# Performance work log

Measured on AMD Instinct MI355X. Metric: run time of the kernel, lower is better.

Reference implementation:

```python
import jax, jax.numpy as jnp
import numpy as np

SIZE_IN = 4096
SIZE_OUT = 8192
EPS = 1e-8  # torch.cosine_similarity default eps


def setup_inputs() -> dict:
    key = jax.random.key(0)
    kx, kw = jax.random.split(key)
    x = jax.random.normal(kx, (4096, SIZE_IN), dtype=jnp.float32)
    # kaiming_uniform_(a=sqrt(5)) -> uniform(-bound, bound), bound = sqrt(6/((1+a^2)*fan_in)) = 1/sqrt(fan_in)
    bound = 1.0 / np.sqrt(SIZE_IN)
    weights = jax.random.uniform(kw, (SIZE_OUT, SIZE_IN), dtype=jnp.float32,
                                 minval=-bound, maxval=bound)
    return {"x": x, "weights": weights}


def reference(x, weights):
    # cosine similarity of each row of x with each weight row, done as one GEMM
    # out[b, o] = <x[b], w[o]> / (max(||x[b]||, eps) * max(||w[o]||, eps))
    x_norm = jnp.maximum(jnp.linalg.norm(x, axis=-1, keepdims=True), EPS)     # [B,1]
    w_norm = jnp.maximum(jnp.linalg.norm(weights, axis=-1), EPS)              # [O]
    dots = jnp.einsum('bi,oi->bo', x, weights)                                # [B,O]
    return dots / (x_norm * w_norm[None, :])
```

## Files before the change

### kernel.cpp

```cpp
#include <hip/hip_runtime.h>
#include <hip/hip_bf16.h>
#include <stdint.h>

#define M_DIM 4096
#define N_DIM 8192
#define K_DIM 4096
#define EPS_F 1e-8f

typedef __attribute__((ext_vector_type(8))) _Float16 f16x8;
typedef __attribute__((ext_vector_type(4))) _Float16 f16x4;
typedef __attribute__((ext_vector_type(4))) float f32x4;

#define GLD16(g, l) __builtin_amdgcn_global_load_lds( \
    (const __attribute__((address_space(1))) void*)(g), \
    (__attribute__((address_space(3))) void*)(l), 16, 0, 0)

#define BARRIER() do { asm volatile("" ::: "memory"); \
  __builtin_amdgcn_s_barrier(); asm volatile("" ::: "memory"); } while (0)

__global__ __launch_bounds__(256) void prep_kernel(
    const float* __restrict__ x, const float* __restrict__ w,
    _Float16* __restrict__ xh, _Float16* __restrict__ wh,
    float* __restrict__ partials) {
  int r = blockIdx.x;
  const float* src;
  _Float16* dst;
  if (r < M_DIM) {
    src = x + (size_t)r * K_DIM;
    dst = xh + (size_t)r * K_DIM;
  } else {
    int rr = r - M_DIM;
    src = w + (size_t)rr * K_DIM;
    dst = wh + (size_t)rr * K_DIM;
  }
  const int lane = threadIdx.x & 63;
  const int wv = threadIdx.x >> 6;
  const int base = wv * 1024;
  float s = 0.f;
#pragma unroll
  for (int i = 0; i < 4; ++i) {
    int c = base + i * 256 + lane * 4;
    float4 v = *(const float4*)(src + c);
    s += v.x * v.x + v.y * v.y + v.z * v.z + v.w * v.w;
    f16x4 h;
    h[0] = (_Float16)v.x; h[1] = (_Float16)v.y;
    h[2] = (_Float16)v.z; h[3] = (_Float16)v.w;
    *(f16x4*)(dst + c) = h;
  }
#pragma unroll
  for (int off = 32; off > 0; off >>= 1) s += __shfl_down(s, off);
  if (lane == 0) partials[r * 4 + wv] = s;
}

__global__ __launch_bounds__(256) void finalize_kernel(
    const float* __restrict__ partials,
    float* __restrict__ rxn, float* __restrict__ rwn) {
  int r = blockIdx.x * 256 + threadIdx.x;
  f32x4 p = *(const f32x4*)(partials + (size_t)r * 4);
  float t = p[0] + p[1] + p[2] + p[3];
  float v = 1.0f / fmaxf(sqrtf(t), EPS_F);
  if (r < M_DIM) rxn[r] = v;
  else rwn[r - M_DIM] = v;
}

__global__ __launch_bounds__(512, 2) void gemm_cos_kernel(
    const _Float16* __restrict__ xh, const _Float16* __restrict__ wh,
    const float* __restrict__ rxn, const float* __restrict__ rwn,
    float* __restrict__ out) {
  __shared__ __align__(16) char lds[131072];

  const int tid = threadIdx.x;
  const int lane = tid & 63;
  const int wid = tid >> 6;
  const int wm = wid >> 2;
  const int wn = wid & 3;

  int bid = blockIdx.x;
  int swz = (bid & 7) * 64 + (bid >> 3);
  const int bm = (swz >> 5) << 8;
  const int bn = (swz & 31) << 8;

  const int srow = tid >> 2;
  const int scsrc = (tid & 3) ^ ((srow >> 1) & 3);
  const size_t a0_off = (size_t)(bm + srow) * K_DIM + scsrc * 8;
  const size_t a1_off = (size_t)(bm + 128 + srow) * K_DIM + scsrc * 8;
  const size_t b0_off = (size_t)(bn + srow) * K_DIM + scsrc * 8;
  const size_t b1_off = (size_t)(bn + 128 + srow) * K_DIM + scsrc * 8;

  char* const lds_my = lds + tid * 16;

  const int j16 = lane >> 4;
  const int arow_base = wm * 128 + (lane & 15);
  const int brow_base = wn * 64 + (lane & 15);

  f32x4 acc[8][4] = {};

  const int NT = K_DIM / 32;

#define STAGE_A(s) do { int s_ = (s); \
    size_t kt_ = (size_t)s_ * 32; \
    char* d_ = lds_my + (size_t)(s_ & 3) * 32768; \
    GLD16(xh + a0_off + kt_, d_); \
    GLD16(xh + a1_off + kt_, d_ + 8192); } while (0)

#define STAGE_B(s) do { int s_ = (s); \
    size_t kt_ = (size_t)s_ * 32; \
    char* d_ = lds_my + (size_t)(s_ & 3) * 32768; \
    GLD16(wh + b0_off + kt_, d_ + 16384); \
    GLD16(wh + b1_off + kt_, d_ + 24576); } while (0)

  STAGE_A(0); STAGE_B(0);
  STAGE_A(1); STAGE_B(1);
  STAGE_A(2); STAGE_B(2);
  asm volatile("s_waitcnt vmcnt(8)" ::: "memory");
  BARRIER();

  for (int T = 0; T < NT; ++T) {
    char* buf = lds + (size_t)(T & 3) * 32768;
    const bool stg = (T + 3 < NT);

    f16x8 af[4], bg[4];

#pragma unroll
    for (int mi = 0; mi < 4; ++mi) {
      int r = arow_base + mi * 16;
      af[mi] = *(const f16x8*)(buf + r * 64 + ((j16 ^ ((r >> 1) & 3)) << 4));
    }
#pragma unroll
    for (int ni = 0; ni < 4; ++ni) {
      int r = brow_base + ni * 16;
      bg[ni] = *(const f16x8*)(buf + 16384 + r * 64 +
                               ((j16 ^ ((r >> 1) & 3)) << 4));
    }
    if (stg) STAGE_A(T + 3);
    BARRIER();
    __builtin_amdgcn_s_setprio(1);
#pragma unroll
    for (int mi = 0; mi < 4; ++mi)
#pragma unroll
      for (int ni = 0; ni < 4; ++ni)
        acc[mi][ni] = __builtin_amdgcn_mfma_f32_16x16x32_f16(
            af[mi], bg[ni], acc[mi][ni], 0, 0, 0);
    __builtin_amdgcn_s_setprio(0);
    BARRIER();

#pragma unroll
    for (int mi = 0; mi < 4; ++mi) {
      int r = arow_base + 64 + mi * 16;
      af[mi] = *(const f16x8*)(buf + r * 64 + ((j16 ^ ((r >> 1) & 3)) << 4));
    }
    if (stg) STAGE_B(T + 3);
    BARRIER();
    __builtin_amdgcn_s_setprio(1);
#pragma unroll
    for (int mi = 0; mi < 4; ++mi)
#pragma unroll
      for (int ni = 0; ni < 4; ++ni)
        acc[4 + mi][ni] = __builtin_amdgcn_mfma_f32_16x16x32_f16(
            af[mi], bg[ni], acc[4 + mi][ni], 0, 0, 0);
    __builtin_amdgcn_s_setprio(0);

    if (T < NT - 3) {
      asm volatile("s_waitcnt vmcnt(8)" ::: "memory");
    } else if (T == NT - 3) {
      asm volatile("s_waitcnt vmcnt(4)" ::: "memory");
    } else if (T == NT - 2) {
      asm volatile("s_waitcnt vmcnt(0)" ::: "memory");
    }
    BARRIER();
  }

  const int ocol = bn + wn * 64 + (lane & 15);
  const int orow0 = bm + wm * 128 + ((lane >> 4) << 2);
  float rw[4];
#pragma unroll
  for (int ni = 0; ni < 4; ++ni) rw[ni] = rwn[ocol + ni * 16];
#pragma unroll
  for (int m = 0; m < 8; ++m) {
#pragma unroll
    for (int jj = 0; jj < 4; ++jj) {
      int r = orow0 + m * 16 + jj;
      float rx = rxn[r];
#pragma unroll
      for (int ni = 0; ni < 4; ++ni)
        out[(size_t)r * N_DIM + ocol + ni * 16] = acc[m][ni][jj] * rx * rw[ni];
    }
  }
#undef STAGE_A
#undef STAGE_B
}

__global__ __launch_bounds__(256) void fb_norms_kernel(
    const float* __restrict__ x, const float* __restrict__ w,
    float* __restrict__ rxn, float* __restrict__ rwn) {
  int r = blockIdx.x;
  const float* src = (r < M_DIM) ? x + (size_t)r * K_DIM
                                 : w + (size_t)(r - M_DIM) * K_DIM;
  float* rn = (r < M_DIM) ? rxn + r : rwn + (r - M_DIM);
  int tid = threadIdx.x;
  float s = 0.f;
#pragma unroll
  for (int i = 0; i < 4; ++i) {
    int c = (i * 256 + tid) * 4;
    float4 v = *(const float4*)(src + c);
    s += v.x * v.x + v.y * v.y + v.z * v.z + v.w * v.w;
  }
#pragma unroll
  for (int off = 32; off > 0; off >>= 1) s += __shfl_down(s, off);
  __shared__ float red[4];
  if ((tid & 63) == 0) red[tid >> 6] = s;
  __syncthreads();
  if (tid == 0) {
    float t = red[0] + red[1] + red[2] + red[3];
    *rn = 1.0f / fmaxf(sqrtf(t), EPS_F);
  }
}

__global__ __launch_bounds__(256) void fb_gemm_kernel(
    const float* __restrict__ x, const float* __restrict__ w,
    const float* __restrict__ rxn, const float* __restrict__ rwn,
    float* __restrict__ out) {
  __shared__ float As[64][17];
  __shared__ float Bs[64][17];
  int bm = blockIdx.y * 64, bn = blockIdx.x * 64;
  int tid = threadIdx.x;
  int tx = tid & 15, ty = tid >> 4;
  float acc[4][4] = {};
  for (int kt = 0; kt < K_DIM; kt += 16) {
#pragma unroll
    for (int i = 0; i < 4; ++i) {
      int e = i * 256 + tid;
      As[e >> 4][e & 15] = x[(size_t)(bm + (e >> 4)) * K_DIM + kt + (e & 15)];
      Bs[e >> 4][e & 15] = w[(size_t)(bn + (e >> 4)) * K_DIM + kt + (e & 15)];
    }
    __syncthreads();
#pragma unroll
    for (int k = 0; k < 16; ++k)
#pragma unroll
      for (int mi = 0; mi < 4; ++mi)
#pragma unroll
        for (int ni = 0; ni < 4; ++ni)
          acc[mi][ni] += As[ty * 4 + mi][k] * Bs[tx * 4 + ni][k];
    __syncthreads();
  }
#pragma unroll
  for (int mi = 0; mi < 4; ++mi) {
    int r = bm + ty * 4 + mi;
    float rx = rxn[r];
#pragma unroll
    for (int ni = 0; ni < 4; ++ni) {
      int c = bn + tx * 4 + ni;
      out[(size_t)r * N_DIM + c] = acc[mi][ni] * rx * rwn[c];
    }
  }
}

extern "C" void kernel_launch(void* const* d_in, const int* in_sizes, int n_in,
                              void* d_out, int out_size, void* d_ws, size_t ws_size,
                              hipStream_t stream) {
  const float* x = (const float*)d_in[0];
  const float* w = (const float*)d_in[1];
  float* out = (float*)d_out;
  char* ws = (char*)d_ws;

  float* rxn = (float*)ws;
  float* rwn = (float*)(ws + (16 << 10));
  float* partials = (float*)(ws + (64 << 10));
  const size_t base = 256 << 10;
  const size_t xelems = (size_t)M_DIM * K_DIM;
  const size_t welems = (size_t)N_DIM * K_DIM;
  const size_t need = base + (xelems + welems) * sizeof(_Float16);

  if (ws_size >= need) {
    _Float16* xh = (_Float16*)(ws + base);
    _Float16* wh = xh + xelems;
    prep_kernel<<<M_DIM + N_DIM, 256, 0, stream>>>(x, w, xh, wh, partials);
    finalize_kernel<<<(M_DIM + N_DIM) / 256, 256, 0, stream>>>(partials, rxn,
                                                               rwn);
    gemm_cos_kernel<<<512, 512, 0, stream>>>(xh, wh, rxn, rwn, out);
  } else {
    fb_norms_kernel<<<M_DIM + N_DIM, 256, 0, stream>>>(x, w, rxn, rwn);
    fb_gemm_kernel<<<dim3(N_DIM / 64, M_DIM / 64), 256, 0, stream>>>(
        x, w, rxn, rwn, out);
  }
}
```

Before: 528.5 us.

## Restructure GEMM main loop into double-buffered 64-wide K tiles with half-step staging

The K loop now processes 64-wide K tiles in two LDS buffers, each split into two 32-wide halves, instead of a 4-deep ring of 32-wide tiles. Global-to-LDS loads for the next tile are issued in quarter pieces across four compute phases, with explicit lgkmcnt waits and sched_barriers before each MFMA block. The aim is to halve loop overhead and vmcnt waits per K element and give the scheduler a fixed order of LDS reads versus MFMAs. The trade-off is a shallower prefetch distance and more barriers per iteration, which could expose memory latency.

Result: no change. 524.4 us (-0.8%).

```diff
diff --git a/kernel.cpp b/kernel.cpp
--- a/kernel.cpp
+++ b/kernel.cpp
@@ -81,93 +81,145 @@
   const int bn = (swz & 31) << 8;
 
   const int srow = tid >> 2;
-  const int scsrc = (tid & 3) ^ ((srow >> 1) & 3);
-  const size_t a0_off = (size_t)(bm + srow) * K_DIM + scsrc * 8;
-  const size_t a1_off = (size_t)(bm + 128 + srow) * K_DIM + scsrc * 8;
-  const size_t b0_off = (size_t)(bn + srow) * K_DIM + scsrc * 8;
-  const size_t b1_off = (size_t)(bn + 128 + srow) * K_DIM + scsrc * 8;
-
-  char* const lds_my = lds + tid * 16;
+  const int jg = (tid & 3) ^ ((tid >> 3) & 3);
+  const size_t aoff0 = (size_t)(bm + srow) * K_DIM + jg * 8;
+  const size_t aoff1 = (size_t)(bm + 128 + srow) * K_DIM + jg * 8;
+  const size_t boff0 = (size_t)(bn + srow) * K_DIM + jg * 8;
+  const size_t boff1 = (size_t)(bn + 128 + srow) * K_DIM + jg * 8;
 
   const int j16 = lane >> 4;
-  const int arow_base = wm * 128 + (lane & 15);
-  const int brow_base = wn * 64 + (lane & 15);
+  const int arb = wm * 128 + (lane & 15);
+  const int brb = wn * 64 + (lane & 15);
 
   f32x4 acc[8][4] = {};
-
-  const int NT = K_DIM / 32;
-
-#define STAGE_A(s) do { int s_ = (s); \
-    size_t kt_ = (size_t)s_ * 32; \
-    char* d_ = lds_my + (size_t)(s_ & 3) * 32768; \
-    GLD16(xh + a0_off + kt_, d_); \
-    GLD16(xh + a1_off + kt_, d_ + 8192); } while (0)
-
-#define STAGE_B(s) do { int s_ = (s); \
-    size_t kt_ = (size_t)s_ * 32; \
-    char* d_ = lds_my + (size_t)(s_ & 3) * 32768; \
-    GLD16(wh + b0_off + kt_, d_ + 16384); \
-    GLD16(wh + b1_off + kt_, d_ + 24576); } while (0)
-
-  STAGE_A(0); STAGE_B(0);
-  STAGE_A(1); STAGE_B(1);
-  STAGE_A(2); STAGE_B(2);
-  asm volatile("s_waitcnt vmcnt(8)" ::: "memory");
+  const int NT = K_DIM / 64;
+
+#define STAGE(ptr, off0, off1, s_, ks_, isB) do { \
+    char* d_ = lds + (size_t)((s_) & 1) * 65536 + (isB) * 32768 + \
+               (ks_) * 16384 + tid * 16; \
+    size_t g_ = (size_t)(s_) * 64 + (ks_) * 32; \
+    GLD16(ptr + off0 + g_, d_); \
+    GLD16(ptr + off1 + g_, d_ + 8192); } while (0)
+
+#define LDSWZ(base_, r_) ((base_) + (r_) * 64 + ((j16 ^ (((r_) >> 1) & 3)) << 4))
+
+  STAGE(xh, aoff0, aoff1, 0, 0, 0);
+  STAGE(wh, boff0, boff1, 0, 0, 1);
+  STAGE(xh, aoff0, aoff1, 0, 1, 0);
+  STAGE(wh, boff0, boff1, 0, 1, 1);
+  STAGE(xh, aoff0, aoff1, 1, 0, 0);
+  STAGE(wh, boff0, boff1, 1, 0, 1);
+  asm volatile("s_waitcnt vmcnt(4)" ::: "memory");
   BARRIER();
 
   for (int T = 0; T < NT; ++T) {
-    char* buf = lds + (size_t)(T & 3) * 32768;
-    const bool stg = (T + 3 < NT);
-
+    char* const bufb = lds + (size_t)(T & 1) * 65536;
     f16x8 af[4], bg[4];
 
-#pragma unroll
-    for (int mi = 0; mi < 4; ++mi) {
-      int r = arow_base + mi * 16;
-      af[mi] = *(const f16x8*)(buf + r * 64 + ((j16 ^ ((r >> 1) & 3)) << 4));
-    }
-#pragma unroll
-    for (int ni = 0; ni < 4; ++ni) {
-      int r = brow_base + ni * 16;
-      bg[ni] = *(const f16x8*)(buf + 16384 + r * 64 +
-                               ((j16 ^ ((r >> 1) & 3)) << 4));
-    }
-    if (stg) STAGE_A(T + 3);
-    BARRIER();
-    __builtin_amdgcn_s_setprio(1);
-#pragma unroll
-    for (int mi = 0; mi < 4; ++mi)
-#pragma unroll
-      for (int ni = 0; ni < 4; ++ni)
-        acc[mi][ni] = __builtin_amdgcn_mfma_f32_16x16x32_f16(
-            af[mi], bg[ni], acc[mi][ni], 0, 0, 0);
-    __builtin_amdgcn_s_setprio(0);
-    BARRIER();
-
-#pragma unroll
-    for (int mi = 0; mi < 4; ++mi) {
-      int r = arow_base + 64 + mi * 16;
-      af[mi] = *(const f16x8*)(buf + r * 64 + ((j16 ^ ((r >> 1) & 3)) << 4));
-    }
-    if (stg) STAGE_B(T + 3);
-    BARRIER();
-    __builtin_amdgcn_s_setprio(1);
-#pragma unroll
-    for (int mi = 0; mi < 4; ++mi)
-#pragma unroll
-      for (int ni = 0; ni < 4; ++ni)
-        acc[4 + mi][ni] = __builtin_amdgcn_mfma_f32_16x16x32_f16(
-            af[mi], bg[ni], acc[4 + mi][ni], 0, 0, 0);
-    __builtin_amdgcn_s_setprio(0);
-
-    if (T < NT - 3) {
-      asm volatile("s_waitcnt vmcnt(8)" ::: "memory");
-    } else if (T == NT - 3) {
-      asm volatile("s_waitcnt vmcnt(4)" ::: "memory");
-    } else if (T == NT - 2) {
-      asm volatile("s_waitcnt vmcnt(0)" ::: "memory");
-    }
-    BARRIER();
+    {
+      char* ab = bufb;
+      char* bb = bufb + 32768;
+#pragma unroll
+      for (int mi = 0; mi < 4; ++mi) {
+        int r = arb + mi * 16;
+        af[mi] = *(const f16x8*)LDSWZ(ab, r);
+      }
+#pragma unroll
+      for (int ni = 0; ni < 4; ++ni) {
+        int r = brb + ni * 16;
+        bg[ni] = *(const f16x8*)LDSWZ(bb, r);
+      }
+      if (T + 1 < NT) STAGE(xh, aoff0, aoff1, T + 1, 1, 0);
+      BARRIER();
+      asm volatile("s_waitcnt lgkmcnt(0)" ::: "memory");
+      __builtin_amdgcn_sched_barrier(0);
+      __builtin_amdgcn_s_setprio(1);
+#pragma unroll
+      for (int mi = 0; mi < 4; ++mi)
+#pragma unroll
+        for (int ni = 0; ni < 4; ++ni)
+          acc[mi][ni] = __builtin_amdgcn_mfma_f32_16x16x32_f16(
+              af[mi], bg[ni], acc[mi][ni], 0, 0, 0);
+      __builtin_amdgcn_s_setprio(0);
+      BARRIER();
+    }
+
+    {
+      char* ab = bufb;
+#pragma unroll
+      for (int mi = 0; mi < 4; ++mi) {
+        int r = arb + 64 + mi * 16;
+        af[mi] = *(const f16x8*)LDSWZ(ab, r);
+      }
+      if (T + 1 < NT) STAGE(wh, boff0, boff1, T + 1, 1, 1);
+      BARRIER();
+      asm volatile("s_waitcnt lgkmcnt(0)" ::: "memory");
+      __builtin_amdgcn_sched_barrier(0);
+      __builtin_amdgcn_s_setprio(1);
+#pragma unroll
+      for (int mi = 0; mi < 4; ++mi)
+#pragma unroll
+        for (int ni = 0; ni < 4; ++ni)
+          acc[4 + mi][ni] = __builtin_amdgcn_mfma_f32_16x16x32_f16(
+              af[mi], bg[ni], acc[4 + mi][ni], 0, 0, 0);
+      __builtin_amdgcn_s_setprio(0);
+      BARRIER();
+    }
+
+    {
+      char* ab = bufb + 16384;
+      char* bb = bufb + 49152;
+#pragma unroll
+      for (int mi = 0; mi < 4; ++mi) {
+        int r = arb + mi * 16;
+        af[mi] = *(const f16x8*)LDSWZ(ab, r);
+      }
+#pragma unroll
+      for (int ni = 0; ni < 4; ++ni) {
+        int r = brb + ni * 16;
+        bg[ni] = *(const f16x8*)LDSWZ(bb, r);
+      }
+      if (T + 2 < NT) STAGE(xh, aoff0, aoff1, T + 2, 0, 0);
+      BARRIER();
+      asm volatile("s_waitcnt lgkmcnt(0)" ::: "memory");
+      __builtin_amdgcn_sched_barrier(0);
+      __builtin_amdgcn_s_setprio(1);
+#pragma unroll
+      for (int mi = 0; mi < 4; ++mi)
+#pragma unroll
+        for (int ni = 0; ni < 4; ++ni)
+          acc[mi][ni] = __builtin_amdgcn_mfma_f32_16x16x32_f16(
+              af[mi], bg[ni], acc[mi][ni], 0, 0, 0);
+      __builtin_amdgcn_s_setprio(0);
+      BARRIER();
+    }
+
+    {
+      char* ab = bufb + 16384;
+#pragma unroll
+      for (int mi = 0; mi < 4; ++mi) {
+        int r = arb + 64 + mi * 16;
+        af[mi] = *(const f16x8*)LDSWZ(ab, r);
+      }
+      if (T + 2 < NT) {
+        STAGE(wh, boff0, boff1, T + 2, 0, 1);
+        asm volatile("s_waitcnt vmcnt(4)" ::: "memory");
+      } else {
+        asm volatile("s_waitcnt vmcnt(0)" ::: "memory");
+      }
+      BARRIER();
+      asm volatile("s_waitcnt lgkmcnt(0)" ::: "memory");
+      __builtin_amdgcn_sched_barrier(0);
+      __builtin_amdgcn_s_setprio(1);
+#pragma unroll
+      for (int mi = 0; mi < 4; ++mi)
+#pragma unroll
+        for (int ni = 0; ni < 4; ++ni)
+          acc[4 + mi][ni] = __builtin_amdgcn_mfma_f32_16x16x32_f16(
+              af[mi], bg[ni], acc[4 + mi][ni], 0, 0, 0);
+      __builtin_amdgcn_s_setprio(0);
+      BARRIER();
+    }
   }
 
   const int ocol = bn + wn * 64 + (lane & 15);
@@ -186,8 +238,8 @@
         out[(size_t)r * N_DIM + ocol + ni * 16] = acc[m][ni][jj] * rx * rw[ni];
     }
   }
-#undef STAGE_A
-#undef STAGE_B
+#undef STAGE
+#undef LDSWZ
 }
 
 __global__ __launch_bounds__(256) void fb_norms_kernel(
```
